# Kernel tuning notes

Hardware: AMD Instinct MI355X
Metric: run time of the kernel (lower is better)

The kernel has to match this reference:

```python
import jax, jax.numpy as jnp
import numpy as np

B, C_FEAT, C_COND, C_KEY, H, W = 4, 256, 256, 32, 64, 64


def setup_inputs() -> dict:
    key = jax.random.key(0)
    ks = jax.random.split(key, 8)
    s = 0.02
    return {
        "features": jax.random.normal(ks[0], (B, C_FEAT, H, W), jnp.float32),
        "conditions": jax.random.normal(ks[1], (B, C_COND, H, W), jnp.float32),
        "Wq": jax.random.normal(ks[2], (C_KEY, C_COND), jnp.float32) * s,
        "bq": jnp.zeros((C_KEY,), jnp.float32),
        "Wk": jax.random.normal(ks[3], (C_KEY, C_FEAT), jnp.float32) * s,
        "bk": jnp.zeros((C_KEY,), jnp.float32),
        "Wv": jax.random.normal(ks[4], (C_FEAT, C_FEAT), jnp.float32) * s,
        "bv": jnp.zeros((C_FEAT,), jnp.float32),
        "gamma": jnp.zeros((1,), jnp.float32),
    }


def reference(features, conditions, Wq, bq, Wk, bk, Wv, bv, gamma):
    b, c, h, w = features.shape
    n = h * w
    feat = features.reshape(b, c, n)            # [B, C, N]
    cond = conditions.reshape(b, cond_c := conditions.shape[1], n)
    # 1x1 convs == per-pixel linear projections
    q = jnp.einsum('kc,bcn->bnk', Wq, cond) + bq          # [B, N, Ck]
    k = jnp.einsum('kc,bcn->bkn', Wk, feat) + bk[:, None]  # [B, Ck, N]
    v = jnp.einsum('oc,bcn->bon', Wv, feat) + bv[:, None]  # [B, C, N]
    energy = jnp.einsum('bik,bkj->bij', q, k)             # [B, N, N]
    attn = jax.nn.softmax(energy, axis=-1)
    out = jnp.einsum('bcj,bij->bci', v, attn)             # [B, C, N]
    out = out.reshape(b, c, h, w)
    return gamma * out + features
```

## Files before the change

### kernel.cpp

```cpp
#include <hip/hip_runtime.h>

typedef __bf16 bf16_t;
typedef __bf16 bf16x2 __attribute__((ext_vector_type(2)));
typedef __bf16 bf16x4 __attribute__((ext_vector_type(4)));
typedef __bf16 bf16x8 __attribute__((ext_vector_type(8)));
typedef float f32x4 __attribute__((ext_vector_type(4)));
typedef unsigned u32;
typedef unsigned u32x4 __attribute__((ext_vector_type(4)));

#define N_PIX 4096
#define CFEAT 256
#define CKEY 32
#define NBATCH 4

#if __has_builtin(__builtin_amdgcn_exp2f)
#define EXP2(x) __builtin_amdgcn_exp2f(x)
#else
#define EXP2(x) exp2f(x)
#endif

static __device__ __forceinline__ f32x4 mfma16(bf16x8 a, bf16x8 b, f32x4 c) {
    return __builtin_amdgcn_mfma_f32_16x16x32_bf16(a, b, c, 0, 0, 0);
}

static __device__ __forceinline__ void glds16(const void* g, void* l) {
    __builtin_amdgcn_global_load_lds(
        (const __attribute__((address_space(1))) void*)g,
        (__attribute__((address_space(3))) void*)l, 16, 0, 0);
}

static __device__ __forceinline__ u32 pk2(float lo, float hi) {
    bf16x2 t; t[0] = (bf16_t)lo; t[1] = (bf16_t)hi;
    return __builtin_bit_cast(u32, t);
}

static __device__ __forceinline__ void xpose4(u32 &x, u32 &y) {
#if __has_builtin(__builtin_amdgcn_permlane32_swap) && __has_builtin(__builtin_amdgcn_permlane16_swap)
    auto r32 = __builtin_amdgcn_permlane32_swap(x, y, false, false);
    auto r16 = __builtin_amdgcn_permlane16_swap(r32[0], r32[1], false, false);
    x = r16[0]; y = r16[1];
#else
    const int lane = threadIdx.x & 63;
    const int g = lane >> 4, ln = lane & 15;
    const int i0 = ln + ((g & 1) << 5);
    const int i2 = i0 + 16;
    u32 xs0 = (u32)__shfl((int)x, i0), ys0 = (u32)__shfl((int)y, i0);
    u32 xs2 = (u32)__shfl((int)x, i2), ys2 = (u32)__shfl((int)y, i2);
    x = (g < 2) ? xs0 : ys0;
    y = (g < 2) ? xs2 : ys2;
#endif
}

static __device__ __forceinline__ void softmax_tile(
    const bf16x8 kf[4], bf16x8 qf, bf16x8 ones,
    f32x4 &accsum, bf16x8 &pa0, bf16x8 &pa1)
{
    f32x4 zero = {0.f, 0.f, 0.f, 0.f};
    f32x4 st[4];
#pragma unroll
    for (int jt = 0; jt < 4; ++jt) st[jt] = mfma16(kf[jt], qf, zero);
    float ex[16];
#pragma unroll
    for (int jt = 0; jt < 4; ++jt)
#pragma unroll
        for (int r = 0; r < 4; ++r) ex[jt * 4 + r] = EXP2(st[jt][r]);
    u32 a0 = pk2(ex[0],  ex[1]),  a1 = pk2(ex[2],  ex[3]);
    u32 b0 = pk2(ex[4],  ex[5]),  b1 = pk2(ex[6],  ex[7]);
    u32 c0 = pk2(ex[8],  ex[9]),  c1 = pk2(ex[10], ex[11]);
    u32 d0 = pk2(ex[12], ex[13]), d1 = pk2(ex[14], ex[15]);
    xpose4(a0, b0); xpose4(a1, b1);
    xpose4(c0, d0); xpose4(c1, d1);
    u32x4 w0 = {a0, a1, b0, b1};
    u32x4 w1 = {c0, c1, d0, d1};
    pa0 = __builtin_bit_cast(bf16x8, w0);
    pa1 = __builtin_bit_cast(bf16x8, w1);
    accsum = mfma16(ones, pa0, accsum);
    accsum = mfma16(ones, pa1, accsum);
}

__global__ __launch_bounds__(256) void projqk_kernel(
    const float* __restrict__ Wq, const float* __restrict__ bq, const float* __restrict__ Xq,
    const float* __restrict__ Wk, const float* __restrict__ bk, const float* __restrict__ Xk,
    bf16_t* __restrict__ Qt, bf16_t* __restrict__ Kt)
{
    __shared__ __attribute__((aligned(16))) bf16_t T[64][40];
    const int lane = threadIdx.x & 63, wave = threadIdx.x >> 6;
    const int g = lane >> 4, ln = lane & 15;
    const bool isK = (blockIdx.y == 1);
    const float* W    = isK ? Wk : Wq;
    const float* bias = isK ? bk : bq;
    const float* X  = (isK ? Xk : Xq) + (size_t)blockIdx.z * CFEAT * N_PIX;
    bf16_t*      Yt = (isK ? Kt : Qt) + (size_t)blockIdx.z * N_PIX * CKEY;
    const float qscale = isK ? 1.0f : 1.4426950408889634f;

    const int m_base = (wave & 1) * 16;
    const int n_loc  = (wave >> 1) * 32;
    const int n_base = blockIdx.x * 64 + n_loc;

    f32x4 zero = {0.f, 0.f, 0.f, 0.f};
    f32x4 acc[2] = {zero, zero};
    for (int k0 = 0; k0 < CFEAT; k0 += 32) {
        bf16x8 a;
        const float* wp = W + (size_t)(m_base + ln) * CFEAT + k0 + g * 8;
#pragma unroll
        for (int j = 0; j < 8; ++j) a[j] = (bf16_t)wp[j];
#pragma unroll
        for (int nt = 0; nt < 2; ++nt) {
            const float* xp = X + (size_t)(k0 + g * 8) * N_PIX + n_base + nt * 16 + ln;
            bf16x8 bfr;
#pragma unroll
            for (int j = 0; j < 8; ++j) bfr[j] = (bf16_t)xp[(size_t)j * N_PIX];
            acc[nt] = mfma16(a, bfr, acc[nt]);
        }
    }
#pragma unroll
    for (int nt = 0; nt < 2; ++nt)
#pragma unroll
        for (int r = 0; r < 4; ++r) {
            const int ck = m_base + g * 4 + r;
            T[n_loc + nt * 16 + ln][ck] = (bf16_t)((acc[nt][r] + bias[ck]) * qscale);
        }
    __syncthreads();
    const int n  = threadIdx.x >> 2;
    const int sg = threadIdx.x & 3;
    bf16x8 row = *(const bf16x8*)&T[n][sg * 8];
    *(bf16x8*)&Yt[(size_t)(blockIdx.x * 64 + n) * CKEY + sg * 8] = row;
}

__global__ __launch_bounds__(256, 4) void projv_kernel(
    const float* __restrict__ W, const float* __restrict__ bias,
    const float* __restrict__ X, bf16_t* __restrict__ V)
{
    const int lane = threadIdx.x & 63, wave = threadIdx.x >> 6;
    const int g = lane >> 4, ln = lane & 15;
    const int b = blockIdx.z;
    const int n_base = blockIdx.x * 32;
    const int c_wave = blockIdx.y * 128 + wave * 32;
    const float* Xb = X + (size_t)b * CFEAT * N_PIX;
    bf16_t*      Vb = V + (size_t)b * CFEAT * N_PIX;

    f32x4 zero = {0.f, 0.f, 0.f, 0.f};
    f32x4 acc[2][2];
#pragma unroll
    for (int mt = 0; mt < 2; ++mt) { acc[mt][0] = zero; acc[mt][1] = zero; }

    for (int k0 = 0; k0 < CFEAT; k0 += 32) {
        bf16x8 bfr[2];
#pragma unroll
        for (int nt = 0; nt < 2; ++nt) {
            const float* xp = Xb + (size_t)(k0 + g * 8) * N_PIX + n_base + nt * 16 + ln;
#pragma unroll
            for (int j = 0; j < 8; ++j) bfr[nt][j] = (bf16_t)xp[(size_t)j * N_PIX];
        }
#pragma unroll
        for (int mt = 0; mt < 2; ++mt) {
            const float* wp = W + (size_t)(c_wave + mt * 16 + ln) * CFEAT + k0 + g * 8;
            bf16x8 a;
#pragma unroll
            for (int j = 0; j < 8; ++j) a[j] = (bf16_t)wp[j];
            acc[mt][0] = mfma16(a, bfr[0], acc[mt][0]);
            acc[mt][1] = mfma16(a, bfr[1], acc[mt][1]);
        }
    }
#pragma unroll
    for (int mt = 0; mt < 2; ++mt)
#pragma unroll
        for (int nt = 0; nt < 2; ++nt)
#pragma unroll
            for (int r = 0; r < 4; ++r) {
                const int m = c_wave + mt * 16 + g * 4 + r;
                const int n = n_base + nt * 16 + ln;
                Vb[(size_t)m * N_PIX + n] = (bf16_t)(acc[mt][nt][r] + bias[m]);
            }
}

__global__ __launch_bounds__(256, 2) void pv_kernel(
    const bf16_t* __restrict__ Qt, const bf16_t* __restrict__ Kt,
    const bf16_t* __restrict__ V,
    const float* __restrict__ features, const float* __restrict__ gamma,
    float* __restrict__ out)
{
    __shared__ __attribute__((aligned(16))) bf16_t Vlds[4][128 * 64];

    const int lane = threadIdx.x & 63, wave = threadIdx.x >> 6;
    const int g = lane >> 4, ln = lane & 15;
    const int b = blockIdx.z;
    const int i_base = blockIdx.y * 64 + wave * 16;
    const int c_base = blockIdx.x * 128;

    const bf16_t* Qb = Qt + (size_t)b * N_PIX * CKEY;
    const bf16_t* Kb = Kt + (size_t)b * N_PIX * CKEY;
    const bf16_t* Vb = V + (size_t)b * CFEAT * N_PIX;

    const int s0 = wave * 256 + lane, s1 = s0 + 64, s2 = s0 + 128, s3 = s0 + 192;
    const int sc0 = s0 >> 3, sj0 = (s0 & 7) ^ (sc0 & 7);
    const int sc1 = s1 >> 3, sj1 = (s1 & 7) ^ (sc1 & 7);
    const int sc2 = s2 >> 3, sj2 = (s2 & 7) ^ (sc2 & 7);
    const int sc3 = s3 >> 3, sj3 = (s3 & 7) ^ (sc3 & 7);
    const bf16_t* vg0 = Vb + (size_t)(c_base + sc0) * N_PIX + sj0 * 8;
    const bf16_t* vg1 = Vb + (size_t)(c_base + sc1) * N_PIX + sj1 * 8;
    const bf16_t* vg2 = Vb + (size_t)(c_base + sc2) * N_PIX + sj2 * 8;
    const bf16_t* vg3 = Vb + (size_t)(c_base + sc3) * N_PIX + sj3 * 8;

    const bf16x8 qf = *(const bf16x8*)&Qb[(size_t)(i_base + ln) * CKEY + g * 8];

    bf16x8 ones;
#pragma unroll
    for (int j = 0; j < 8; ++j) ones[j] = (bf16_t)1.0f;

    f32x4 zero = {0.f, 0.f, 0.f, 0.f};
    f32x4 acc[8] = {zero, zero, zero, zero, zero, zero, zero, zero};
    f32x4 accsum = zero;

    bf16x8 kfA[4], kfB[4];
    bf16x8 pa0c, pa1c;

    {
        bf16x8 kf0[4];
#pragma unroll
        for (int jt = 0; jt < 4; ++jt)
            kf0[jt] = *(const bf16x8*)&Kb[(size_t)(jt * 16 + ln) * CKEY + g * 8];
        asm volatile("" ::: "memory");
        glds16(vg0, &Vlds[0][wave * 2048]);
        glds16(vg1, &Vlds[0][wave * 2048 + 512]);
        glds16(vg2, &Vlds[0][wave * 2048 + 1024]);
        glds16(vg3, &Vlds[0][wave * 2048 + 1536]);
        glds16(vg0 + 64, &Vlds[1][wave * 2048]);
        glds16(vg1 + 64, &Vlds[1][wave * 2048 + 512]);
        glds16(vg2 + 64, &Vlds[1][wave * 2048 + 1024]);
        glds16(vg3 + 64, &Vlds[1][wave * 2048 + 1536]);
#pragma unroll
        for (int jt = 0; jt < 4; ++jt)
            kfA[jt] = *(const bf16x8*)&Kb[(size_t)(64 + jt * 16 + ln) * CKEY + g * 8];
        softmax_tile(kf0, qf, ones, accsum, pa0c, pa1c);
        asm volatile("s_waitcnt vmcnt(8)" ::: "memory");
        __builtin_amdgcn_s_barrier();
        asm volatile("" ::: "memory");
    }

#define PV_ITER(NN, KFU, KFN)                                                  \
  {                                                                            \
    const int nn = (NN);                                                       \
    const bf16_t* Vt = &Vlds[nn & 3][0];                                       \
    bf16x8 vfl[8];                                                             \
    _Pragma("unroll")                                                          \
    for (int ct = 0; ct < 4; ++ct) {                                           \
      const int c = ct * 16 + ln;                                              \
      vfl[2 * ct]     = *(const bf16x8*)&Vt[(c * 8 + ( g      ^ (c & 7))) * 8];\
      vfl[2 * ct + 1] = *(const bf16x8*)&Vt[(c * 8 + ((4 + g) ^ (c & 7))) * 8];\
    }                                                                          \
    const int jq2 = ((nn + 2) & 63) * 64;                                      \
    _Pragma("unroll")                                                          \
    for (int jt = 0; jt < 4; ++jt)                                             \
      KFN[jt] = *(const bf16x8*)&Kb[(size_t)(jq2 + jt * 16 + ln) * CKEY + g * 8]; \
    asm volatile("" ::: "memory");     \
    const int jn = (nn * 64 + 128) & (N_PIX - 1);                              \
    bf16_t* ldst = &Vlds[(nn + 2) & 3][wave * 2048];                           \
    glds16(vg0 + jn, ldst);                                                    \
    glds16(vg1 + jn, ldst + 512);                                              \
    glds16(vg2 + jn, ldst + 1024);                                             \
    glds16(vg3 + jn, ldst + 1536);                                             \
    bf16x8 pa0n, pa1n;                                                         \
    const bool live = (nn < 63);                                               \
    if (live) softmax_tile(KFU, qf, ones, accsum, pa0n, pa1n);                 \
    asm volatile("s_waitcnt vmcnt(8)" ::: "memory");                           \
    __builtin_amdgcn_s_barrier();                                              \
    asm volatile("" ::: "memory");                                             \
    bf16x8 vfh[8];                                                             \
    _Pragma("unroll")                                                          \
    for (int ct = 4; ct < 8; ++ct) {                                           \
      const int c = ct * 16 + ln;                                              \
      vfh[2 * (ct - 4)]     = *(const bf16x8*)&Vt[(c * 8 + ( g      ^ (c & 7))) * 8]; \
      vfh[2 * (ct - 4) + 1] = *(const bf16x8*)&Vt[(c * 8 + ((4 + g) ^ (c & 7))) * 8]; \
    }                                                                          \
    _Pragma("unroll")                                                          \
    for (int ct = 0; ct < 4; ++ct) {                                           \
      acc[ct] = mfma16(vfl[2 * ct],     pa0c, acc[ct]);                        \
      acc[ct] = mfma16(vfl[2 * ct + 1], pa1c, acc[ct]);                        \
    }                                                                          \
    _Pragma("unroll")                                                          \
    for (int ct = 0; ct < 4; ++ct) {                                           \
      acc[4 + ct] = mfma16(vfh[2 * ct],     pa0c, acc[4 + ct]);                \
      acc[4 + ct] = mfma16(vfh[2 * ct + 1], pa1c, acc[4 + ct]);                \
    }                                                                          \
    if (live) { pa0c = pa0n; pa1c = pa1n; }                                    \
  }

    for (int n2 = 0; n2 < 32; ++n2) {
        PV_ITER(2 * n2,     kfA, kfB);
        PV_ITER(2 * n2 + 1, kfB, kfA);
    }
#undef PV_ITER

    const float s_lane = gamma[0] / accsum[0];

#pragma unroll
    for (int ct = 0; ct < 8; ++ct)
#pragma unroll
        for (int r = 0; r < 4; ++r) {
            const int c = c_base + ct * 16 + g * 4 + r;
            const int i = i_base + ln;
            const size_t idx = ((size_t)b * CFEAT + c) * N_PIX + i;
            out[idx] = s_lane * acc[ct][r] + features[idx];
        }
}

extern "C" void kernel_launch(void* const* d_in, const int* in_sizes, int n_in,
                              void* d_out, int out_size, void* d_ws, size_t ws_size,
                              hipStream_t stream) {
    const float* features   = (const float*)d_in[0];
    const float* conditions = (const float*)d_in[1];
    const float* Wq  = (const float*)d_in[2];
    const float* bq  = (const float*)d_in[3];
    const float* Wk  = (const float*)d_in[4];
    const float* bk  = (const float*)d_in[5];
    const float* Wv  = (const float*)d_in[6];
    const float* bv  = (const float*)d_in[7];
    const float* gam = (const float*)d_in[8];
    float* out = (float*)d_out;

    bf16_t* Qt = (bf16_t*)d_ws;
    bf16_t* Kt = Qt + (size_t)NBATCH * N_PIX * CKEY;
    bf16_t* Vw = Kt + (size_t)NBATCH * N_PIX * CKEY;

    projqk_kernel<<<dim3(N_PIX / 64, 2, NBATCH), 256, 0, stream>>>(
        Wq, bq, conditions, Wk, bk, features, Qt, Kt);
    projv_kernel<<<dim3(N_PIX / 32, 2, NBATCH), 256, 0, stream>>>(Wv, bv, features, Vw);
    pv_kernel<<<dim3(2, N_PIX / 64, NBATCH), 256, 0, stream>>>(
        Qt, Kt, Vw, features, gam, out);
}
```

Baseline: 172.8 us.

## Merge Q/K/V projection kernels into one launch and hoist V LDS reads with setprio

Combines the separate QK and V projection kernels into a single launch of 1024 blocks. The first 512 blocks compute Q/K and the rest compute V, with each wave now covering 64 output channels so one block spans all 256 channels. This removes one kernel launch, and each V block reads its feature tile once instead of twice. In the PV loop, all 16 V fragments are loaded from LDS before the barrier, and the MFMA burst is wrapped in s_setprio. The cost is higher register pressure in both kernels and a V branch that may occupy the GPU less evenly than the Q/K branch.

```diff
diff --git a/kernel.cpp b/kernel.cpp
--- a/kernel.cpp
+++ b/kernel.cpp
@@ -78,100 +78,102 @@
     accsum = mfma16(ones, pa1, accsum);
 }
 
-__global__ __launch_bounds__(256) void projqk_kernel(
-    const float* __restrict__ Wq, const float* __restrict__ bq, const float* __restrict__ Xq,
-    const float* __restrict__ Wk, const float* __restrict__ bk, const float* __restrict__ Xk,
-    bf16_t* __restrict__ Qt, bf16_t* __restrict__ Kt)
+__global__ __launch_bounds__(256) void proj_kernel(
+    const float* __restrict__ Wq, const float* __restrict__ bq, const float* __restrict__ cond,
+    const float* __restrict__ Wk, const float* __restrict__ bk, const float* __restrict__ feat,
+    const float* __restrict__ Wv, const float* __restrict__ bv,
+    bf16_t* __restrict__ Qt, bf16_t* __restrict__ Kt, bf16_t* __restrict__ Vv)
 {
     __shared__ __attribute__((aligned(16))) bf16_t T[64][40];
     const int lane = threadIdx.x & 63, wave = threadIdx.x >> 6;
     const int g = lane >> 4, ln = lane & 15;
-    const bool isK = (blockIdx.y == 1);
-    const float* W    = isK ? Wk : Wq;
-    const float* bias = isK ? bk : bq;
-    const float* X  = (isK ? Xk : Xq) + (size_t)blockIdx.z * CFEAT * N_PIX;
-    bf16_t*      Yt = (isK ? Kt : Qt) + (size_t)blockIdx.z * N_PIX * CKEY;
-    const float qscale = isK ? 1.0f : 1.4426950408889634f;
-
-    const int m_base = (wave & 1) * 16;
-    const int n_loc  = (wave >> 1) * 32;
-    const int n_base = blockIdx.x * 64 + n_loc;
-
+    const int bid = blockIdx.x;
     f32x4 zero = {0.f, 0.f, 0.f, 0.f};
-    f32x4 acc[2] = {zero, zero};
-    for (int k0 = 0; k0 < CFEAT; k0 += 32) {
-        bf16x8 a;
-        const float* wp = W + (size_t)(m_base + ln) * CFEAT + k0 + g * 8;
-#pragma unroll
-        for (int j = 0; j < 8; ++j) a[j] = (bf16_t)wp[j];
-#pragma unroll
-        for (int nt = 0; nt < 2; ++nt) {
-            const float* xp = X + (size_t)(k0 + g * 8) * N_PIX + n_base + nt * 16 + ln;
-            bf16x8 bfr;
-#pragma unroll
-            for (int j = 0; j < 8; ++j) bfr[j] = (bf16_t)xp[(size_t)j * N_PIX];
-            acc[nt] = mfma16(a, bfr, acc[nt]);
+
+    if (bid < 512) {
+        const bool isK = (bid >= 256);
+        const int idx = bid & 255;
+        const int xt = idx & 63;
+        const int b  = idx >> 6;
+        const float* W    = isK ? Wk : Wq;
+        const float* bias = isK ? bk : bq;
+        const float* X  = (isK ? feat : cond) + (size_t)b * CFEAT * N_PIX;
+        bf16_t*      Yt = (isK ? Kt : Qt) + (size_t)b * N_PIX * CKEY;
+        const float qscale = isK ? 1.0f : 1.4426950408889634f;
+
+        const int m_base = (wave & 1) * 16;
+        const int n_loc  = (wave >> 1) * 32;
+        const int n_base = xt * 64 + n_loc;
+
+        f32x4 acc[2] = {zero, zero};
+        for (int k0 = 0; k0 < CFEAT; k0 += 32) {
+            bf16x8 a;
+            const float* wp = W + (size_t)(m_base + ln) * CFEAT + k0 + g * 8;
+#pragma unroll
+            for (int j = 0; j < 8; ++j) a[j] = (bf16_t)wp[j];
+#pragma unroll
+            for (int nt = 0; nt < 2; ++nt) {
+                const float* xp = X + (size_t)(k0 + g * 8) * N_PIX + n_base + nt * 16 + ln;
+                bf16x8 bfr;
+#pragma unroll
+                for (int j = 0; j < 8; ++j) bfr[j] = (bf16_t)xp[(size_t)j * N_PIX];
+                acc[nt] = mfma16(a, bfr, acc[nt]);
+            }
         }
+#pragma unroll
+        for (int nt = 0; nt < 2; ++nt)
+#pragma unroll
+            for (int r = 0; r < 4; ++r) {
+                const int ck = m_base + g * 4 + r;
+                T[n_loc + nt * 16 + ln][ck] = (bf16_t)((acc[nt][r] + bias[ck]) * qscale);
+            }
+        __syncthreads();
+        const int n  = threadIdx.x >> 2;
+        const int sg = threadIdx.x & 3;
+        bf16x8 row = *(const bf16x8*)&T[n][sg * 8];
+        *(bf16x8*)&Yt[(size_t)(xt * 64 + n) * CKEY + sg * 8] = row;
+    } else {
+        const int idx = bid - 512;
+        const int xt = idx & 127;
+        const int b  = idx >> 7;
+        const int n_base = xt * 32;
+        const int c_wave = wave * 64;
+        const float* Xb = feat + (size_t)b * CFEAT * N_PIX;
+        bf16_t*      Vb = Vv + (size_t)b * CFEAT * N_PIX;
+
+        f32x4 acc[4][2];
+#pragma unroll
+        for (int mt = 0; mt < 4; ++mt) { acc[mt][0] = zero; acc[mt][1] = zero; }
+
+        for (int k0 = 0; k0 < CFEAT; k0 += 32) {
+            bf16x8 bfr[2];
+#pragma unroll
+            for (int nt = 0; nt < 2; ++nt) {
+                const float* xp = Xb + (size_t)(k0 + g * 8) * N_PIX + n_base + nt * 16 + ln;
+#pragma unroll
+                for (int j = 0; j < 8; ++j) bfr[nt][j] = (bf16_t)xp[(size_t)j * N_PIX];
+            }
+#pragma unroll
+            for (int mt = 0; mt < 4; ++mt) {
+                const float* wp = Wv + (size_t)(c_wave + mt * 16 + ln) * CFEAT + k0 + g * 8;
+                bf16x8 a;
+#pragma unroll
+                for (int j = 0; j < 8; ++j) a[j] = (bf16_t)wp[j];
+                acc[mt][0] = mfma16(a, bfr[0], acc[mt][0]);
+                acc[mt][1] = mfma16(a, bfr[1], acc[mt][1]);
+            }
+        }
+#pragma unroll
+        for (int mt = 0; mt < 4; ++mt)
+#pragma unroll
+            for (int nt = 0; nt < 2; ++nt)
+#pragma unroll
+                for (int r = 0; r < 4; ++r) {
+                    const int m = c_wave + mt * 16 + g * 4 + r;
+                    const int n = n_base + nt * 16 + ln;
+                    Vb[(size_t)m * N_PIX + n] = (bf16_t)(acc[mt][nt][r] + bv[m]);
+                }
     }
-#pragma unroll
-    for (int nt = 0; nt < 2; ++nt)
-#pragma unroll
-        for (int r = 0; r < 4; ++r) {
-            const int ck = m_base + g * 4 + r;
-            T[n_loc + nt * 16 + ln][ck] = (bf16_t)((acc[nt][r] + bias[ck]) * qscale);
-        }
-    __syncthreads();
-    const int n  = threadIdx.x >> 2;
-    const int sg = threadIdx.x & 3;
-    bf16x8 row = *(const bf16x8*)&T[n][sg * 8];
-    *(bf16x8*)&Yt[(size_t)(blockIdx.x * 64 + n) * CKEY + sg * 8] = row;
-}
-
-__global__ __launch_bounds__(256, 4) void projv_kernel(
-    const float* __restrict__ W, const float* __restrict__ bias,
-    const float* __restrict__ X, bf16_t* __restrict__ V)
-{
-    const int lane = threadIdx.x & 63, wave = threadIdx.x >> 6;
-    const int g = lane >> 4, ln = lane & 15;
-    const int b = blockIdx.z;
-    const int n_base = blockIdx.x * 32;
-    const int c_wave = blockIdx.y * 128 + wave * 32;
-    const float* Xb = X + (size_t)b * CFEAT * N_PIX;
-    bf16_t*      Vb = V + (size_t)b * CFEAT * N_PIX;
-
-    f32x4 zero = {0.f, 0.f, 0.f, 0.f};
-    f32x4 acc[2][2];
-#pragma unroll
-    for (int mt = 0; mt < 2; ++mt) { acc[mt][0] = zero; acc[mt][1] = zero; }
-
-    for (int k0 = 0; k0 < CFEAT; k0 += 32) {
-        bf16x8 bfr[2];
-#pragma unroll
-        for (int nt = 0; nt < 2; ++nt) {
-            const float* xp = Xb + (size_t)(k0 + g * 8) * N_PIX + n_base + nt * 16 + ln;
-#pragma unroll
-            for (int j = 0; j < 8; ++j) bfr[nt][j] = (bf16_t)xp[(size_t)j * N_PIX];
-        }
-#pragma unroll
-        for (int mt = 0; mt < 2; ++mt) {
-            const float* wp = W + (size_t)(c_wave + mt * 16 + ln) * CFEAT + k0 + g * 8;
-            bf16x8 a;
-#pragma unroll
-            for (int j = 0; j < 8; ++j) a[j] = (bf16_t)wp[j];
-            acc[mt][0] = mfma16(a, bfr[0], acc[mt][0]);
-            acc[mt][1] = mfma16(a, bfr[1], acc[mt][1]);
-        }
-    }
-#pragma unroll
-    for (int mt = 0; mt < 2; ++mt)
-#pragma unroll
-        for (int nt = 0; nt < 2; ++nt)
-#pragma unroll
-            for (int r = 0; r < 4; ++r) {
-                const int m = c_wave + mt * 16 + g * 4 + r;
-                const int n = n_base + nt * 16 + ln;
-                Vb[(size_t)m * N_PIX + n] = (bf16_t)(acc[mt][nt][r] + bias[m]);
-            }
 }
 
 __global__ __launch_bounds__(256, 2) void pv_kernel(
@@ -242,12 +244,12 @@
   {                                                                            \
     const int nn = (NN);                                                       \
     const bf16_t* Vt = &Vlds[nn & 3][0];                                       \
-    bf16x8 vfl[8];                                                             \
+    bf16x8 vf[16];                                                             \
     _Pragma("unroll")                                                          \
-    for (int ct = 0; ct < 4; ++ct) {                                           \
+    for (int ct = 0; ct < 8; ++ct) {                                           \
       const int c = ct * 16 + ln;                                              \
-      vfl[2 * ct]     = *(const bf16x8*)&Vt[(c * 8 + ( g      ^ (c & 7))) * 8];\
-      vfl[2 * ct + 1] = *(const bf16x8*)&Vt[(c * 8 + ((4 + g) ^ (c & 7))) * 8];\
+      vf[2 * ct]     = *(const bf16x8*)&Vt[(c * 8 + ( g      ^ (c & 7))) * 8]; \
+      vf[2 * ct + 1] = *(const bf16x8*)&Vt[(c * 8 + ((4 + g) ^ (c & 7))) * 8]; \
     }                                                                          \
     const int jq2 = ((nn + 2) & 63) * 64;                                      \
     _Pragma("unroll")                                                          \
@@ -266,23 +268,13 @@
     asm volatile("s_waitcnt vmcnt(8)" ::: "memory");                           \
     __builtin_amdgcn_s_barrier();                                              \
     asm volatile("" ::: "memory");                                             \
-    bf16x8 vfh[8];                                                             \
+    __builtin_amdgcn_s_setprio(1);                                             \
     _Pragma("unroll")                                                          \
-    for (int ct = 4; ct < 8; ++ct) {                                           \
-      const int c = ct * 16 + ln;                                              \
-      vfh[2 * (ct - 4)]     = *(const bf16x8*)&Vt[(c * 8 + ( g      ^ (c & 7))) * 8]; \
-      vfh[2 * (ct - 4) + 1] = *(const bf16x8*)&Vt[(c * 8 + ((4 + g) ^ (c & 7))) * 8]; \
+    for (int ct = 0; ct < 8; ++ct) {                                           \
+      acc[ct] = mfma16(vf[2 * ct],     pa0c, acc[ct]);                         \
+      acc[ct] = mfma16(vf[2 * ct + 1], pa1c, acc[ct]);                         \
     }                                                                          \
-    _Pragma("unroll")                                                          \
-    for (int ct = 0; ct < 4; ++ct) {                                           \
-      acc[ct] = mfma16(vfl[2 * ct],     pa0c, acc[ct]);                        \
-      acc[ct] = mfma16(vfl[2 * ct + 1], pa1c, acc[ct]);                        \
-    }                                                                          \
-    _Pragma("unroll")                                                          \
-    for (int ct = 0; ct < 4; ++ct) {                                           \
-      acc[4 + ct] = mfma16(vfh[2 * ct],     pa0c, acc[4 + ct]);                \
-      acc[4 + ct] = mfma16(vfh[2 * ct + 1], pa1c, acc[4 + ct]);                \
-    }                                                                          \
+    __builtin_amdgcn_s_setprio(0);                                             \
     if (live) { pa0c = pa0n; pa1c = pa1n; }                                    \
   }
 
@@ -323,9 +315,8 @@
     bf16_t* Kt = Qt + (size_t)NBATCH * N_PIX * CKEY;
     bf16_t* Vw = Kt + (size_t)NBATCH * N_PIX * CKEY;
 
-    projqk_kernel<<<dim3(N_PIX / 64, 2, NBATCH), 256, 0, stream>>>(
-        Wq, bq, conditions, Wk, bk, features, Qt, Kt);
-    projv_kernel<<<dim3(N_PIX / 32, 2, NBATCH), 256, 0, stream>>>(Wv, bv, features, Vw);
+    proj_kernel<<<dim3(1024, 1, 1), 256, 0, stream>>>(
+        Wq, bq, conditions, Wk, bk, features, Wv, bv, Qt, Kt, Vw);
     pv_kernel<<<dim3(2, N_PIX / 64, NBATCH), 256, 0, stream>>>(
         Qt, Kt, Vw, features, gam, out);
 }
```

Result: faster. 169.4 us (-2.0%).
